# Optimization experiments

Hardware: AMD Instinct MI355X
Metric: run time of the kernel (lower is better)

## Reference

```python
import jax, jax.numpy as jnp
import numpy as np


def conv(x, w, stride=1, pad=0):
    return jax.lax.conv_general_dilated(
        x, w, (stride, stride), [(pad, pad), (pad, pad)],
        dimension_numbers=('NCHW', 'OIHW', 'NCHW'))


def group_norm(x, scale, bias, groups=32, eps=1e-5):
    B, C, H, W = x.shape
    xg = x.reshape(B, groups, C // groups, H, W)
    m = xg.mean(axis=(2, 3, 4), keepdims=True)
    v = xg.var(axis=(2, 3, 4), keepdims=True)
    xn = ((xg - m) * jax.lax.rsqrt(v + eps)).reshape(B, C, H, W)
    return xn * scale[None, :, None, None] + bias[None, :, None, None]


def bilinear_sample(x, py, px):
    # x: [B,C,H,W]; py, px: [B,K,Ho,Wo] absolute sampling coords.
    # Returns [B,C,K,Ho,Wo]; out-of-bounds corners contribute zero
    # (matches deform-conv CUDA kernel semantics).
    B, C, H, W = x.shape
    y0 = jnp.floor(py)
    x0 = jnp.floor(px)
    wy1 = py - y0
    wx1 = px - x0
    xf = x.reshape(B, C, H * W)
    Ksp = py.shape[1:]

    def corner(yi, xi, wy, wx):
        valid = (yi >= 0) & (yi < H) & (xi >= 0) & (xi < W)
        yc = jnp.clip(yi, 0, H - 1).astype(jnp.int32)
        xc = jnp.clip(xi, 0, W - 1).astype(jnp.int32)
        idx = (yc * W + xc).reshape(B, 1, -1)          # [B,1,K*Ho*Wo]
        v = jnp.take_along_axis(xf, idx, axis=2).reshape(B, C, *Ksp)
        w = (wy * wx * valid).astype(x.dtype)[:, None]  # [B,1,K,Ho,Wo]
        return v * w

    return (corner(y0, x0, 1.0 - wy1, 1.0 - wx1)
            + corner(y0, x0 + 1, 1.0 - wy1, wx1)
            + corner(y0 + 1, x0, wy1, 1.0 - wx1)
            + corner(y0 + 1, x0 + 1, wy1, wx1))


def setup_inputs() -> dict:
    key = jax.random.key(0)
    ks = jax.random.split(key, 8)
    B, Cin, H, W = 4, 1024, 64, 64
    Cb = 256  # bottleneck channels
    x = jax.random.normal(ks[0], (B, Cin, H, W), dtype=jnp.float32)
    w1 = jax.random.normal(ks[1], (Cb, Cin, 1, 1), dtype=jnp.float32) * (1.0 / np.sqrt(Cin))
    w_off = jax.random.normal(ks[2], (27, Cb, 3, 3), dtype=jnp.float32) * 0.01
    b_off = jnp.zeros((27,), dtype=jnp.float32)
    w2 = jax.random.normal(ks[3], (Cb, Cb, 3, 3), dtype=jnp.float32) * (1.0 / np.sqrt(Cb * 9))
    w3 = jax.random.normal(ks[4], (Cin, Cb, 1, 1), dtype=jnp.float32) * (1.0 / np.sqrt(Cb))
    return {
        'x': x,
        'w1': w1, 'gn1_scale': jnp.ones((Cb,), jnp.float32), 'gn1_bias': jnp.zeros((Cb,), jnp.float32),
        'w_off': w_off, 'b_off': b_off,
        'w2': w2, 'gn2_scale': jnp.ones((Cb,), jnp.float32), 'gn2_bias': jnp.zeros((Cb,), jnp.float32),
        'w3': w3, 'gn3_scale': jnp.ones((Cin,), jnp.float32), 'gn3_bias': jnp.zeros((Cin,), jnp.float32),
        'stride': 4,
    }


def reference(x, w1, gn1_scale, gn1_bias, w_off, b_off, w2, gn2_scale, gn2_bias,
              w3, gn3_scale, gn3_bias, stride):
    # stride only selects the offset-conv / norm bank (single bank here).
    out = conv(x, w1)                                   # 1x1
    out = jax.nn.relu(group_norm(out, gn1_scale, gn1_bias))

    om = conv(out, w_off, pad=1) + b_off[None, :, None, None]  # [B,27,H,W]
    K = 9
    off_x = om[:, :K]
    off_y = om[:, K:2 * K]
    mask = jax.nn.sigmoid(om[:, 2 * K:])                # [B,9,H,W]

    B, C, H, W = out.shape
    ky, kx = jnp.meshgrid(jnp.arange(3), jnp.arange(3), indexing='ij')
    ky = (ky.reshape(K) - 1).astype(om.dtype)           # kernel taps, pad=1, dil=1
    kx = (kx.reshape(K) - 1).astype(om.dtype)
    grid_y = jnp.arange(H, dtype=om.dtype)[None, :, None] + ky[:, None, None]  # [9,H,1]
    grid_x = jnp.arange(W, dtype=om.dtype)[None, None, :] + kx[:, None, None]  # [9,1,W]
    py = grid_y[None] + off_y                           # [B,9,H,W]
    px = grid_x[None] + off_x

    sampled = bilinear_sample(out, py, px) * mask[:, None]      # [B,C,9,H,W]
    out = jnp.einsum('bckhw,ock->bohw', sampled, w2.reshape(w2.shape[0], w2.shape[1], K))
    out = jax.nn.relu(group_norm(out, gn2_scale, gn2_bias))

    out = conv(out, w3)                                 # 1x1
    out = group_norm(out, gn3_scale, gn3_bias)
    return jax.nn.relu(out + x)
```

## Files before the change

### kernel.cpp

```cpp
#include <hip/hip_runtime.h>
#include <math.h>

#define BATCH 4
#define CIN   1024
#define CB    256
#define HH    64
#define WW    64
#define PP    4096
#define EPSV  1e-5f

using shortx8 = __attribute__((ext_vector_type(8))) short;
using floatx4 = __attribute__((ext_vector_type(4))) float;
using intx4   = __attribute__((ext_vector_type(4))) int;

static __device__ inline unsigned short f2bf(float f) {
    unsigned int u = __float_as_uint(f);
    u += 0x7fffu + ((u >> 16) & 1u);
    return (unsigned short)(u >> 16);
}
static __device__ inline float bf2f(unsigned short s) {
    return __uint_as_float(((unsigned int)s) << 16);
}
static __device__ inline float bflo(unsigned int u) {
    return __uint_as_float(u << 16);
}
static __device__ inline float bfhi(unsigned int u) {
    return __uint_as_float(u & 0xffff0000u);
}

__global__ __launch_bounds__(256)
void gemm_bf16(const unsigned short* __restrict__ A,
               const unsigned short* __restrict__ BTg,
               float* __restrict__ Cg, int M, int N, int K) {
    const int b = blockIdx.z;
    const unsigned short* BT = BTg + (size_t)b * N * K;
    float* C = Cg + (size_t)b * M * N;
    const int m0 = blockIdx.y * 128;
    const int n0 = blockIdx.x * 128;
    const int tid = threadIdx.x;
    const int lane = tid & 63;
    const int wid = tid >> 6;
    const int l15 = lane & 15;
    const int quad = lane >> 4;

    __shared__ __align__(16) unsigned short As[128 * 40];
    __shared__ __align__(16) unsigned short Bs[128 * 40];

    floatx4 acc[2][8];
#pragma unroll
    for (int i = 0; i < 2; i++)
#pragma unroll
        for (int j = 0; j < 8; j++) acc[i][j] = (floatx4){0.f, 0.f, 0.f, 0.f};

    const int row = tid >> 1;
    const int half = tid & 1;

    for (int k0 = 0; k0 < K; k0 += 32) {
        const unsigned short* ga = A + (size_t)(m0 + row) * K + k0 + half * 16;
        const unsigned short* gb = BT + (size_t)(n0 + row) * K + k0 + half * 16;
        float4 a0 = *(const float4*)ga;
        float4 a1 = *(const float4*)(ga + 8);
        float4 b0 = *(const float4*)gb;
        float4 b1 = *(const float4*)(gb + 8);
        __syncthreads();
        *(float4*)((char*)As + row * 80 + half * 32) = a0;
        *(float4*)((char*)As + row * 80 + half * 32 + 16) = a1;
        *(float4*)((char*)Bs + row * 80 + half * 32) = b0;
        *(float4*)((char*)Bs + row * 80 + half * 32 + 16) = b1;
        __syncthreads();
        shortx8 af[2], bf[8];
#pragma unroll
        for (int i = 0; i < 2; i++)
            af[i] = *(const shortx8*)((const char*)As +
                    (wid * 32 + 16 * i + l15) * 80 + quad * 16);
#pragma unroll
        for (int j = 0; j < 8; j++)
            bf[j] = *(const shortx8*)((const char*)Bs +
                    (16 * j + l15) * 80 + quad * 16);
#pragma unroll
        for (int i = 0; i < 2; i++)
#pragma unroll
            for (int j = 0; j < 8; j++)
                acc[i][j] = __builtin_amdgcn_mfma_f32_16x16x32_bf16(
                    af[i], bf[j], acc[i][j], 0, 0, 0);
    }

#pragma unroll
    for (int i = 0; i < 2; i++) {
#pragma unroll
        for (int r = 0; r < 4; r++) {
            int m = m0 + wid * 32 + 16 * i + quad * 4 + r;
            float* dst = C + (size_t)m * N + n0 + l15;
#pragma unroll
            for (int j = 0; j < 8; j++)
                dst[16 * j] = acc[i][j][r];
        }
    }
}

__global__ __launch_bounds__(256)
void transp_bf16(const float* __restrict__ src, unsigned short* __restrict__ dst,
                 int C, int P) {
    const int p0 = blockIdx.x * 64;
    const int c0 = blockIdx.y * 64;
    const int b = blockIdx.z;
    __shared__ unsigned short t[64][72];
    const float* s = src + ((size_t)b * C + c0) * P + p0;
    for (int e = threadIdx.x; e < 4096; e += 256) {
        int r = e >> 6, col = e & 63;
        t[r][col] = f2bf(s[(size_t)r * P + col]);
    }
    __syncthreads();
    unsigned short* d = dst + ((size_t)b * P + p0) * C + c0;
    for (int u = threadIdx.x; u < 512; u += 256) {
        int pr = u >> 3, c8 = (u & 7) * 8;
        ushort4 v0, v1;
        v0.x = t[c8 + 0][pr]; v0.y = t[c8 + 1][pr];
        v0.z = t[c8 + 2][pr]; v0.w = t[c8 + 3][pr];
        v1.x = t[c8 + 4][pr]; v1.y = t[c8 + 5][pr];
        v1.z = t[c8 + 6][pr]; v1.w = t[c8 + 7][pr];
        *(ushort4*)&d[(size_t)pr * C + c8] = v0;
        *(ushort4*)&d[(size_t)pr * C + c8 + 4] = v1;
    }
}

__global__ __launch_bounds__(256)
void gn2t(const float* __restrict__ src, const float2* __restrict__ st,
          const float* __restrict__ sc, const float* __restrict__ bi,
          unsigned short* __restrict__ dst) {
    const int p0 = blockIdx.x * 64;
    const int c0 = blockIdx.y * 64;
    const int b = blockIdx.z;
    __shared__ unsigned short t[64][72];
    const float* s = src + ((size_t)b * CB + c0) * PP + p0;
    for (int e = threadIdx.x; e < 4096; e += 256) {
        int r = e >> 6, col = e & 63;
        int c = c0 + r;
        float2 m = st[b * 32 + (c >> 3)];
        float a = m.y * sc[c];
        float bb = bi[c] - m.x * a;
        t[r][col] = f2bf(fmaxf(s[(size_t)r * PP + col] * a + bb, 0.f));
    }
    __syncthreads();
    unsigned short* d = dst + ((size_t)b * PP + p0) * CB + c0;
    for (int u = threadIdx.x; u < 512; u += 256) {
        int pr = u >> 3, c8 = (u & 7) * 8;
        ushort4 v0, v1;
        v0.x = t[c8 + 0][pr]; v0.y = t[c8 + 1][pr];
        v0.z = t[c8 + 2][pr]; v0.w = t[c8 + 3][pr];
        v1.x = t[c8 + 4][pr]; v1.y = t[c8 + 5][pr];
        v1.z = t[c8 + 6][pr]; v1.w = t[c8 + 7][pr];
        *(ushort4*)&d[(size_t)pr * CB + c8] = v0;
        *(ushort4*)&d[(size_t)pr * CB + c8 + 4] = v1;
    }
}

__global__ __launch_bounds__(256)
void cvt_bf16(const float* __restrict__ s, unsigned short* __restrict__ d, int n) {
    int i = blockIdx.x * 256 + threadIdx.x;
    if (i < n) d[i] = f2bf(s[i]);
}

__global__ __launch_bounds__(256)
void gn_stats_part(const float* __restrict__ src, float2* __restrict__ part,
                   int C, int Cpg) {
    int bgs = blockIdx.x;
    int bg = bgs >> 2, s = bgs & 3;
    int b = bg >> 5, g = bg & 31;
    const float* base = src + ((size_t)b * C + (size_t)g * Cpg) * PP;
    int n4 = (Cpg * PP) >> 2;
    int per = n4 >> 2;
    const float4* p4 = (const float4*)base + (size_t)s * per;
    float sm = 0.f, ss = 0.f;
    for (int i = threadIdx.x; i < per; i += 256) {
        float4 v = p4[i];
        sm += v.x + v.y + v.z + v.w;
        ss += v.x * v.x + v.y * v.y + v.z * v.z + v.w * v.w;
    }
    for (int off = 32; off > 0; off >>= 1) {
        sm += __shfl_down(sm, off, 64);
        ss += __shfl_down(ss, off, 64);
    }
    __shared__ float rs[4], rss[4];
    int lane = threadIdx.x & 63, wid = threadIdx.x >> 6;
    if (lane == 0) { rs[wid] = sm; rss[wid] = ss; }
    __syncthreads();
    if (threadIdx.x == 0)
        part[bgs] = make_float2(rs[0] + rs[1] + rs[2] + rs[3],
                                rss[0] + rss[1] + rss[2] + rss[3]);
}

__global__ __launch_bounds__(128)
void gn_stats_fin(const float2* __restrict__ part, float2* __restrict__ stats,
                  int cnt) {
    int bg = threadIdx.x;
    float2 p0 = part[bg * 4 + 0], p1 = part[bg * 4 + 1];
    float2 p2 = part[bg * 4 + 2], p3 = part[bg * 4 + 3];
    float S  = p0.x + p1.x + p2.x + p3.x;
    float SS = p0.y + p1.y + p2.y + p3.y;
    float mean = S / (float)cnt;
    float var = SS / (float)cnt - mean * mean;
    stats[bg] = make_float2(mean, rsqrtf(var + EPSV));
}

__global__ __launch_bounds__(256)
void woff_conv(const float* __restrict__ w_off, unsigned short* __restrict__ wobf) {
    int t = blockIdx.x * 256 + threadIdx.x;
    if (t >= 32 * 2304) return;
    int m = t / 2304;
    int r = t - m * 2304;
    int tap = r >> 8, c = r & 255;
    float v = (m < 27) ? w_off[((size_t)m * 256 + c) * 9 + tap] : 0.f;
    wobf[t] = f2bf(v);
}

__global__ __launch_bounds__(256)
void conv_off_mfma(const unsigned short* __restrict__ bfAT,
                   const unsigned short* __restrict__ wobf,
                   const float* __restrict__ boff,
                   float* __restrict__ om) {
    const int blk = blockIdx.x;
    const int xcd = blk & 7;
    const int b = xcd >> 1;
    const int tile = ((blk >> 3) << 1) | (xcd & 1);
    const int p0 = tile * 32;
    const int tid = threadIdx.x;
    const int lane = tid & 63;
    const int wid = tid >> 6;
    const int l15 = lane & 15;
    const int quad = lane >> 4;
    const int mh = (wid >> 1) << 4;
    const int ph = (wid & 1) << 4;

    __shared__ __align__(16) unsigned short Bs[8 * 1288];

    const int y0r = p0 >> 6;
    const int x0 = p0 & 63;
    const unsigned short* xb = bfAT + ((size_t)b << 20);
    const unsigned short* arow = wobf + (size_t)(mh + l15) * 2304 + quad * 8;

    floatx4 acc = (floatx4){0.f, 0.f, 0.f, 0.f};

    for (int tap = 0; tap < 9; ++tap) {
        const int dy = tap / 3 - 1, dx = tap % 3 - 1;
        const int yy = y0r + dy;
        const bool rowok = (yy >= 0 && yy < 64);
        __syncthreads();
        for (int e = tid; e < 1024; e += 256) {
            int px = e >> 5, ck = e & 31;
            int xx = x0 + px + dx;
            uint4 v = make_uint4(0u, 0u, 0u, 0u);
            if (rowok && xx >= 0 && xx < 64) {
                int srow = (yy << 6) + xx;
                v = *(const uint4*)(xb + ((size_t)srow << 8) + ck * 8);
            }
            *(uint4*)((char*)Bs + (ck >> 2) * 2576 + px * 80 + (ck & 3) * 16) = v;
        }
        __syncthreads();
        const unsigned short* at = arow + tap * 256;
#pragma unroll
        for (int cc = 0; cc < 8; ++cc) {
            shortx8 af = *(const shortx8*)(at + cc * 32);
            shortx8 bf = *(const shortx8*)((const char*)Bs + cc * 2576 +
                         (ph + l15) * 80 + quad * 16);
            acc = __builtin_amdgcn_mfma_f32_16x16x32_bf16(af, bf, acc, 0, 0, 0);
        }
    }

#pragma unroll
    for (int r = 0; r < 4; ++r) {
        int m = mh + quad * 4 + r;
        if (m < 27)
            om[((size_t)b * 27 + m) * PP + p0 + ph + l15] = acc[r] + boff[m];
    }
}

__global__ __launch_bounds__(512, 2)
void gemm2_mfma(const unsigned short* __restrict__ bfAT,
                const unsigned short* __restrict__ w2bf,
                const float* __restrict__ om, float* __restrict__ out2) {
    const int blk = blockIdx.x;
    const int xcd = blk & 7;
    const int b = xcd >> 1;
    const int p0 = (((blk >> 3) << 1) | (xcd & 1)) * 64;
    const int tid = threadIdx.x;
    const int lane = tid & 63;
    const int wid = tid >> 6;
    const int l15 = lane & 15;
    const int quad = lane >> 4;

    __shared__ __align__(16) unsigned short As0[256 * 40];
    __shared__ __align__(16) unsigned short As1[256 * 40];
    __shared__ __align__(16) unsigned short Bs0[64 * 40];
    __shared__ __align__(16) unsigned short Bs1[64 * 40];
    __shared__ float sw0[576], sw1[576], sw2[576], sw3[576];
    __shared__ int   si0[576], si1[576];

    const float* ob = om + (size_t)b * 27 * PP;
    for (int e = tid; e < 576; e += 512) {
        int k = e >> 6, p = e & 63;
        int pg = p0 + p;
        float offx = ob[(size_t)k * PP + pg];
        float offy = ob[(size_t)(9 + k) * PP + pg];
        float ms = 1.f / (1.f + expf(-ob[(size_t)(18 + k) * PP + pg]));
        int y = pg >> 6, x = pg & 63;
        float py = (float)(y + k / 3 - 1) + offy;
        float px = (float)(x + (k % 3) - 1) + offx;
        float y0f = floorf(py), x0f = floorf(px);
        float wy1 = py - y0f, wx1 = px - x0f;
        int iy0 = (int)y0f, ix0 = (int)x0f;
        int iy1 = iy0 + 1;
        float wy0v = (iy0 >= 0 && iy0 < 64) ? (1.f - wy1) * ms : 0.f;
        float wy1v = (iy1 >= 0 && iy1 < 64) ? wy1 * ms : 0.f;
        int cy0 = min(max(iy0, 0), 63), cy1 = min(max(iy1, 0), 63);
        float xa, xb; int q;
        if (ix0 >= 0 && ix0 <= 62)      { q = ix0; xa = 1.f - wx1; xb = wx1;       }
        else if (ix0 == -1)             { q = 0;   xa = wx1;       xb = 0.f;       }
        else if (ix0 == 63)             { q = 62;  xa = 0.f;       xb = 1.f - wx1; }
        else                            { q = 0;   xa = 0.f;       xb = 0.f;       }
        sw0[e] = wy0v * xa;
        sw1[e] = wy0v * xb;
        sw2[e] = wy1v * xa;
        sw3[e] = wy1v * xb;
        si0[e] = (cy0 << 6) + q;
        si1[e] = (cy1 << 6) + q;
    }

    floatx4 acc[2][4];
#pragma unroll
    for (int i = 0; i < 2; i++)
#pragma unroll
        for (int j = 0; j < 4; j++) acc[i][j] = (floatx4){0.f, 0.f, 0.f, 0.f};

    const int cq = tid & 7;
    const int bp = tid >> 3;
    const int so = tid >> 1;
    const int sh = tid & 1;
    const unsigned short* xbase = bfAT + (((size_t)b) << 20);
    const unsigned short* abase = w2bf + (size_t)so * 2304 + sh * 32;
    const unsigned short* gbq = xbase + cq * 8;
    const int mbase = wid * 32;

    __syncthreads();

    float4 a0, a1, a2, a3;
    uint4 v00, v01, v10, v11;
    float w0, w1, w2v, w3v;
    {
        a0 = ((const float4*)abase)[0];
        a1 = ((const float4*)abase)[1];
        a2 = ((const float4*)abase)[2];
        a3 = ((const float4*)abase)[3];
        int tix = bp;
        w0 = sw0[tix]; w1 = sw1[tix]; w2v = sw2[tix]; w3v = sw3[tix];
        int r0 = si0[tix], r1 = si1[tix];
        v00 = *(const uint4*)(gbq + ((size_t)r0 << 8));
        v01 = *(const uint4*)(gbq + ((size_t)(r0 + 1) << 8));
        v10 = *(const uint4*)(gbq + ((size_t)r1 << 8));
        v11 = *(const uint4*)(gbq + ((size_t)(r1 + 1) << 8));
    }

    int tap = 0, cc2 = 0;
    for (int seg = 0; seg < 36; ++seg) {
        float f0 = w0 * bflo(v00.x) + w1 * bflo(v01.x)
                 + w2v * bflo(v10.x) + w3v * bflo(v11.x);
        float f1 = w0 * bfhi(v00.x) + w1 * bfhi(v01.x)
                 + w2v * bfhi(v10.x) + w3v * bfhi(v11.x);
        float f2 = w0 * bflo(v00.y) + w1 * bflo(v01.y)
                 + w2v * bflo(v10.y) + w3v * bflo(v11.y);
        float f3 = w0 * bfhi(v00.y) + w1 * bfhi(v01.y)
                 + w2v * bfhi(v10.y) + w3v * bfhi(v11.y);
        float f4 = w0 * bflo(v00.z) + w1 * bflo(v01.z)
                 + w2v * bflo(v10.z) + w3v * bflo(v11.z);
        float f5 = w0 * bfhi(v00.z) + w1 * bfhi(v01.z)
                 + w2v * bfhi(v10.z) + w3v * bfhi(v11.z);
        float f6 = w0 * bflo(v00.w) + w1 * bflo(v01.w)
                 + w2v * bflo(v10.w) + w3v * bflo(v11.w);
        float f7 = w0 * bfhi(v00.w) + w1 * bfhi(v01.w)
                 + w2v * bfhi(v10.w) + w3v * bfhi(v11.w);
        uint4 bw;
        bw.x = (unsigned int)f2bf(f0) | ((unsigned int)f2bf(f1) << 16);
        bw.y = (unsigned int)f2bf(f2) | ((unsigned int)f2bf(f3) << 16);
        bw.z = (unsigned int)f2bf(f4) | ((unsigned int)f2bf(f5) << 16);
        bw.w = (unsigned int)f2bf(f6) | ((unsigned int)f2bf(f7) << 16);
        unsigned short* adst = sh ? As1 : As0;
        *(float4*)((char*)adst + so * 80 +  0) = a0;
        *(float4*)((char*)adst + so * 80 + 16) = a1;
        *(float4*)((char*)adst + so * 80 + 32) = a2;
        *(float4*)((char*)adst + so * 80 + 48) = a3;
        unsigned short* bdst = (cq & 4) ? Bs1 : Bs0;
        *(uint4*)((char*)bdst + bp * 80 + (cq & 3) * 16) = bw;
        __syncthreads();

        int ntap = tap + 1, ncc2 = cc2;
        if (ntap == 9) { ntap = 0; ncc2 = (cc2 + 1) & 3; }
        {
            const unsigned short* gsrc = abase + ntap * 256 + ncc2 * 64;
            a0 = ((const float4*)gsrc)[0];
            a1 = ((const float4*)gsrc)[1];
            a2 = ((const float4*)gsrc)[2];
            a3 = ((const float4*)gsrc)[3];
            int tix = ntap * 64 + bp;
            int r0 = si0[tix], r1 = si1[tix];
            const unsigned short* gb = gbq + ncc2 * 64;
            v00 = *(const uint4*)(gb + ((size_t)r0 << 8));
            v01 = *(const uint4*)(gb + ((size_t)(r0 + 1) << 8));
            v10 = *(const uint4*)(gb + ((size_t)r1 << 8));
            v11 = *(const uint4*)(gb + ((size_t)(r1 + 1) << 8));
            w0 = sw0[tix]; w1 = sw1[tix]; w2v = sw2[tix]; w3v = sw3[tix];
        }

        shortx8 af[2][2], bfr[2][4];
#pragma unroll
        for (int i = 0; i < 2; i++) {
            af[0][i] = *(const shortx8*)((const char*)As0 +
                       (mbase + 16 * i + l15) * 80 + quad * 16);
            af[1][i] = *(const shortx8*)((const char*)As1 +
                       (mbase + 16 * i + l15) * 80 + quad * 16);
        }
#pragma unroll
        for (int j = 0; j < 4; j++) {
            bfr[0][j] = *(const shortx8*)((const char*)Bs0 +
                        (16 * j + l15) * 80 + quad * 16);
            bfr[1][j] = *(const shortx8*)((const char*)Bs1 +
                        (16 * j + l15) * 80 + quad * 16);
        }
#pragma unroll
        for (int ks = 0; ks < 2; ks++)
#pragma unroll
            for (int i = 0; i < 2; i++)
#pragma unroll
                for (int j = 0; j < 4; j++)
                    acc[i][j] = __builtin_amdgcn_mfma_f32_16x16x32_bf16(
                        af[ks][i], bfr[ks][j], acc[i][j], 0, 0, 0);
        __syncthreads();
        tap = ntap; cc2 = ncc2;
    }

    const size_t chbase = ((size_t)b * CB) << 12;
#pragma unroll
    for (int i = 0; i < 2; i++) {
#pragma unroll
        for (int r = 0; r < 4; r++) {
            int row = mbase + 16 * i + quad * 4 + r;
            float* dst = out2 + chbase + ((size_t)row << 12) + p0 + l15;
#pragma unroll
            for (int j = 0; j < 4; j++)
                dst[16 * j] = acc[i][j][r];
        }
    }
}

__global__ __launch_bounds__(256)
void w2conv(const float* __restrict__ w2, unsigned short* __restrict__ w2bf) {
    int t = blockIdx.x * 256 + threadIdx.x;
    if (t >= 256 * 2304) return;
    int o = t / 2304;
    int r = t - o * 2304;
    int tap = r >> 8, c = r & 255;
    w2bf[t] = f2bf(w2[((size_t)o * 256 + c) * 9 + tap]);
}

__global__ __launch_bounds__(256)
void final_k(float* __restrict__ dout, const float* __restrict__ x,
             const float2* __restrict__ stats, const float* __restrict__ sc,
             const float* __restrict__ bi) {
    long i = (long)blockIdx.x * 256 + threadIdx.x;
    long total4 = ((long)BATCH * CIN * PP) >> 2;
    if (i >= total4) return;
    long e = i << 2;
    int c = (int)((e >> 12) & 1023);
    int b = (int)(e >> 22);
    float2 st = stats[b * 32 + (c >> 5)];
    float a = st.y * sc[c];
    float bb = bi[c] - st.x * a;
    float4 v = ((float4*)dout)[i];
    float4 xv = ((const float4*)x)[i];
    v.x = fmaxf(v.x * a + bb + xv.x, 0.f);
    v.y = fmaxf(v.y * a + bb + xv.y, 0.f);
    v.z = fmaxf(v.z * a + bb + xv.z, 0.f);
    v.w = fmaxf(v.w * a + bb + xv.w, 0.f);
    ((float4*)dout)[i] = v;
}

extern "C" void kernel_launch(void* const* d_in, const int* in_sizes, int n_in,
                              void* d_out, int out_size, void* d_ws, size_t ws_size,
                              hipStream_t stream) {
    const float* x   = (const float*)d_in[0];
    const float* w1  = (const float*)d_in[1];
    const float* g1s = (const float*)d_in[2];
    const float* g1b = (const float*)d_in[3];
    const float* wof = (const float*)d_in[4];
    const float* bof = (const float*)d_in[5];
    const float* w2  = (const float*)d_in[6];
    const float* g2s = (const float*)d_in[7];
    const float* g2b = (const float*)d_in[8];
    const float* w3  = (const float*)d_in[9];
    const float* g3s = (const float*)d_in[10];
    const float* g3b = (const float*)d_in[11];
    float* out = (float*)d_out;

    float* ws = (float*)d_ws;
    unsigned short* w1bf   = (unsigned short*)(ws + 0);
    float*          out1r  = ws + 131072;
    float*          out2   = ws + 131072;
    unsigned short* xbfT   = (unsigned short*)(ws + 4325376);
    unsigned short* bfAT   = (unsigned short*)(ws + 6422528);
    float*          om     = ws + 8519680;
    unsigned short* w2bf   = (unsigned short*)(ws + 8962048);
    unsigned short* wobf   = (unsigned short*)(ws + 9256960);
    unsigned short* out2bT = (unsigned short*)(ws + 4325376);
    unsigned short* w3bf   = (unsigned short*)(ws + 11354112);
    float2* st1  = (float2*)(ws + 11485184);
    float2* st2  = st1 + 128;
    float2* st3  = st2 + 128;
    float2* part = st3 + 128;

    transp_bf16<<<dim3(64, 16, 4), 256, 0, stream>>>(x, xbfT, 1024, 4096);
    cvt_bf16<<<1024, 256, 0, stream>>>(w1, w1bf, 262144);
    gemm_bf16<<<dim3(32, 2, 4), 256, 0, stream>>>(w1bf, xbfT, out1r, 256, 4096, 1024);
    gn_stats_part<<<512, 256, 0, stream>>>(out1r, part, 256, 8);
    gn_stats_fin<<<1, 128, 0, stream>>>(part, st1, 8 * PP);
    gn2t<<<dim3(64, 4, 4), 256, 0, stream>>>(out1r, st1, g1s, g1b, bfAT);
    woff_conv<<<288, 256, 0, stream>>>(wof, wobf);
    conv_off_mfma<<<512, 256, 0, stream>>>(bfAT, wobf, bof, om);
    w2conv<<<2304, 256, 0, stream>>>(w2, w2bf);
    cvt_bf16<<<1024, 256, 0, stream>>>(w3, w3bf, 262144);
    gemm2_mfma<<<dim3(256, 1, 1), 512, 0, stream>>>(bfAT, w2bf, om, out2);
    gn_stats_part<<<512, 256, 0, stream>>>(out2, part, 256, 8);
    gn_stats_fin<<<1, 128, 0, stream>>>(part, st2, 8 * PP);
    gn2t<<<dim3(64, 4, 4), 256, 0, stream>>>(out2, st2, g2s, g2b, out2bT);
    gemm_bf16<<<dim3(32, 8, 4), 256, 0, stream>>>(w3bf, out2bT, out, 1024, 4096, 256);
    gn_stats_part<<<512, 256, 0, stream>>>(out, part, 1024, 32);
    gn_stats_fin<<<1, 128, 0, stream>>>(part, st3, 32 * PP);
    final_k<<<16384, 256, 0, stream>>>(out, x, st3, g3s, g3b);
}
```

Baseline: 348.8 us.

## Fuse GroupNorm statistics into GEMM epilogues and load gemm2 A operand directly to registers

Result: no change. 352.1 us (+1.0%).

```diff
diff --git a/kernel.cpp b/kernel.cpp
--- a/kernel.cpp
+++ b/kernel.cpp
@@ -11,7 +11,6 @@
 
 using shortx8 = __attribute__((ext_vector_type(8))) short;
 using floatx4 = __attribute__((ext_vector_type(4))) float;
-using intx4   = __attribute__((ext_vector_type(4))) int;
 
 static __device__ inline unsigned short f2bf(float f) {
     unsigned int u = __float_as_uint(f);
@@ -31,7 +30,8 @@
 __global__ __launch_bounds__(256)
 void gemm_bf16(const unsigned short* __restrict__ A,
                const unsigned short* __restrict__ BTg,
-               float* __restrict__ Cg, int M, int N, int K) {
+               float* __restrict__ Cg, int M, int N, int K,
+               float* __restrict__ pS, float* __restrict__ pSS, int gshift) {
     const int b = blockIdx.z;
     const unsigned short* BT = BTg + (size_t)b * N * K;
     float* C = Cg + (size_t)b * M * N;
@@ -45,6 +45,8 @@
 
     __shared__ __align__(16) unsigned short As[128 * 40];
     __shared__ __align__(16) unsigned short Bs[128 * 40];
+    __shared__ float sgs[32], sgss[32];
+    if (tid < 32) { sgs[tid] = 0.f; sgss[tid] = 0.f; }
 
     floatx4 acc[2][8];
 #pragma unroll
@@ -91,10 +93,29 @@
         for (int r = 0; r < 4; r++) {
             int m = m0 + wid * 32 + 16 * i + quad * 4 + r;
             float* dst = C + (size_t)m * N + n0 + l15;
-#pragma unroll
-            for (int j = 0; j < 8; j++)
-                dst[16 * j] = acc[i][j][r];
+            float s = 0.f, ss = 0.f;
+#pragma unroll
+            for (int j = 0; j < 8; j++) {
+                float v = acc[i][j][r];
+                dst[16 * j] = v;
+                s += v; ss += v * v;
+            }
+#pragma unroll
+            for (int off = 1; off < 16; off <<= 1) {
+                s  += __shfl_xor(s, off, 64);
+                ss += __shfl_xor(ss, off, 64);
+            }
+            if (l15 == 0) {
+                int g = (m >> gshift) & 31;
+                atomicAdd(&sgs[g], s);
+                atomicAdd(&sgss[g], ss);
+            }
         }
+    }
+    __syncthreads();
+    if (tid < 32) {
+        atomicAdd(&pS[b * 32 + tid], sgs[tid]);
+        atomicAdd(&pSS[b * 32 + tid], sgss[tid]);
     }
 }
 
@@ -161,43 +182,11 @@
     if (i < n) d[i] = f2bf(s[i]);
 }
 
-__global__ __launch_bounds__(256)
-void gn_stats_part(const float* __restrict__ src, float2* __restrict__ part,
-                   int C, int Cpg) {
-    int bgs = blockIdx.x;
-    int bg = bgs >> 2, s = bgs & 3;
-    int b = bg >> 5, g = bg & 31;
-    const float* base = src + ((size_t)b * C + (size_t)g * Cpg) * PP;
-    int n4 = (Cpg * PP) >> 2;
-    int per = n4 >> 2;
-    const float4* p4 = (const float4*)base + (size_t)s * per;
-    float sm = 0.f, ss = 0.f;
-    for (int i = threadIdx.x; i < per; i += 256) {
-        float4 v = p4[i];
-        sm += v.x + v.y + v.z + v.w;
-        ss += v.x * v.x + v.y * v.y + v.z * v.z + v.w * v.w;
-    }
-    for (int off = 32; off > 0; off >>= 1) {
-        sm += __shfl_down(sm, off, 64);
-        ss += __shfl_down(ss, off, 64);
-    }
-    __shared__ float rs[4], rss[4];
-    int lane = threadIdx.x & 63, wid = threadIdx.x >> 6;
-    if (lane == 0) { rs[wid] = sm; rss[wid] = ss; }
-    __syncthreads();
-    if (threadIdx.x == 0)
-        part[bgs] = make_float2(rs[0] + rs[1] + rs[2] + rs[3],
-                                rss[0] + rss[1] + rss[2] + rss[3]);
-}
-
 __global__ __launch_bounds__(128)
-void gn_stats_fin(const float2* __restrict__ part, float2* __restrict__ stats,
-                  int cnt) {
+void gn_stats_fin(const float* __restrict__ pS, const float* __restrict__ pSS,
+                  float2* __restrict__ stats, int cnt) {
     int bg = threadIdx.x;
-    float2 p0 = part[bg * 4 + 0], p1 = part[bg * 4 + 1];
-    float2 p2 = part[bg * 4 + 2], p3 = part[bg * 4 + 3];
-    float S  = p0.x + p1.x + p2.x + p3.x;
-    float SS = p0.y + p1.y + p2.y + p3.y;
+    float S = pS[bg], SS = pSS[bg];
     float mean = S / (float)cnt;
     float var = SS / (float)cnt - mean * mean;
     stats[bg] = make_float2(mean, rsqrtf(var + EPSV));
@@ -278,7 +267,8 @@
 __global__ __launch_bounds__(512, 2)
 void gemm2_mfma(const unsigned short* __restrict__ bfAT,
                 const unsigned short* __restrict__ w2bf,
-                const float* __restrict__ om, float* __restrict__ out2) {
+                const float* __restrict__ om, float* __restrict__ out2,
+                float* __restrict__ pS, float* __restrict__ pSS) {
     const int blk = blockIdx.x;
     const int xcd = blk & 7;
     const int b = xcd >> 1;
@@ -289,12 +279,12 @@
     const int l15 = lane & 15;
     const int quad = lane >> 4;
 
-    __shared__ __align__(16) unsigned short As0[256 * 40];
-    __shared__ __align__(16) unsigned short As1[256 * 40];
     __shared__ __align__(16) unsigned short Bs0[64 * 40];
     __shared__ __align__(16) unsigned short Bs1[64 * 40];
     __shared__ float sw0[576], sw1[576], sw2[576], sw3[576];
     __shared__ int   si0[576], si1[576];
+    __shared__ float sgs[32], sgss[32];
+    if (tid < 32) { sgs[tid] = 0.f; sgss[tid] = 0.f; }
 
     const float* ob = om + (size_t)b * 27 * PP;
     for (int e = tid; e < 576; e += 512) {
@@ -334,23 +324,22 @@
 
     const int cq = tid & 7;
     const int bp = tid >> 3;
-    const int so = tid >> 1;
-    const int sh = tid & 1;
     const unsigned short* xbase = bfAT + (((size_t)b) << 20);
-    const unsigned short* abase = w2bf + (size_t)so * 2304 + sh * 32;
     const unsigned short* gbq = xbase + cq * 8;
     const int mbase = wid * 32;
+    const unsigned short* afb = w2bf + (size_t)(mbase + l15) * 2304 + quad * 8;
 
     __syncthreads();
 
-    float4 a0, a1, a2, a3;
+    shortx8 afc[2][2];
     uint4 v00, v01, v10, v11;
     float w0, w1, w2v, w3v;
     {
-        a0 = ((const float4*)abase)[0];
-        a1 = ((const float4*)abase)[1];
-        a2 = ((const float4*)abase)[2];
-        a3 = ((const float4*)abase)[3];
+#pragma unroll
+        for (int ks = 0; ks < 2; ks++)
+#pragma unroll
+            for (int i = 0; i < 2; i++)
+                afc[ks][i] = *(const shortx8*)(afb + (size_t)i * 36864 + ks * 32);
         int tix = bp;
         w0 = sw0[tix]; w1 = sw1[tix]; w2v = sw2[tix]; w3v = sw3[tix];
         int r0 = si0[tix], r1 = si1[tix];
@@ -383,23 +372,20 @@
         bw.y = (unsigned int)f2bf(f2) | ((unsigned int)f2bf(f3) << 16);
         bw.z = (unsigned int)f2bf(f4) | ((unsigned int)f2bf(f5) << 16);
         bw.w = (unsigned int)f2bf(f6) | ((unsigned int)f2bf(f7) << 16);
-        unsigned short* adst = sh ? As1 : As0;
-        *(float4*)((char*)adst + so * 80 +  0) = a0;
-        *(float4*)((char*)adst + so * 80 + 16) = a1;
-        *(float4*)((char*)adst + so * 80 + 32) = a2;
-        *(float4*)((char*)adst + so * 80 + 48) = a3;
         unsigned short* bdst = (cq & 4) ? Bs1 : Bs0;
         *(uint4*)((char*)bdst + bp * 80 + (cq & 3) * 16) = bw;
         __syncthreads();
 
         int ntap = tap + 1, ncc2 = cc2;
         if (ntap == 9) { ntap = 0; ncc2 = (cc2 + 1) & 3; }
+        shortx8 afn[2][2];
         {
-            const unsigned short* gsrc = abase + ntap * 256 + ncc2 * 64;
-            a0 = ((const float4*)gsrc)[0];
-            a1 = ((const float4*)gsrc)[1];
-            a2 = ((const float4*)gsrc)[2];
-            a3 = ((const float4*)gsrc)[3];
+            const unsigned short* ab = afb + ntap * 256 + ncc2 * 64;
+#pragma unroll
+            for (int ks = 0; ks < 2; ks++)
+#pragma unroll
+                for (int i = 0; i < 2; i++)
+                    afn[ks][i] = *(const shortx8*)(ab + (size_t)i * 36864 + ks * 32);
             int tix = ntap * 64 + bp;
             int r0 = si0[tix], r1 = si1[tix];
             const unsigned short* gb = gbq + ncc2 * 64;
@@ -410,14 +396,7 @@
             w0 = sw0[tix]; w1 = sw1[tix]; w2v = sw2[tix]; w3v = sw3[tix];
         }
 
-        shortx8 af[2][2], bfr[2][4];
-#pragma unroll
-        for (int i = 0; i < 2; i++) {
-            af[0][i] = *(const shortx8*)((const char*)As0 +
-                       (mbase + 16 * i + l15) * 80 + quad * 16);
-            af[1][i] = *(const shortx8*)((const char*)As1 +
-                       (mbase + 16 * i + l15) * 80 + quad * 16);
-        }
+        shortx8 bfr[2][4];
 #pragma unroll
         for (int j = 0; j < 4; j++) {
             bfr[0][j] = *(const shortx8*)((const char*)Bs0 +
@@ -432,8 +411,13 @@
 #pragma unroll
                 for (int j = 0; j < 4; j++)
                     acc[i][j] = __builtin_amdgcn_mfma_f32_16x16x32_bf16(
-                        af[ks][i], bfr[ks][j], acc[i][j], 0, 0, 0);
+                        afc[ks][i], bfr[ks][j], acc[i][j], 0, 0, 0);
         __syncthreads();
+#pragma unroll
+        for (int ks = 0; ks < 2; ks++)
+#pragma unroll
+            for (int i = 0; i < 2; i++)
+                afc[ks][i] = afn[ks][i];
         tap = ntap; cc2 = ncc2;
     }
 
@@ -444,10 +428,29 @@
         for (int r = 0; r < 4; r++) {
             int row = mbase + 16 * i + quad * 4 + r;
             float* dst = out2 + chbase + ((size_t)row << 12) + p0 + l15;
-#pragma unroll
-            for (int j = 0; j < 4; j++)
-                dst[16 * j] = acc[i][j][r];
+            float s = 0.f, ss = 0.f;
+#pragma unroll
+            for (int j = 0; j < 4; j++) {
+                float v = acc[i][j][r];
+                dst[16 * j] = v;
+                s += v; ss += v * v;
+            }
+#pragma unroll
+            for (int off = 1; off < 16; off <<= 1) {
+                s  += __shfl_xor(s, off, 64);
+                ss += __shfl_xor(ss, off, 64);
+            }
+            if (l15 == 0) {
+                int g = row >> 3;
+                atomicAdd(&sgs[g], s);
+                atomicAdd(&sgss[g], ss);
+            }
         }
+    }
+    __syncthreads();
+    if (tid < 32) {
+        atomicAdd(&pS[b * 32 + tid], sgs[tid]);
+        atomicAdd(&pSS[b * 32 + tid], sgss[tid]);
     }
 }
 
@@ -514,24 +517,28 @@
     float2* st1  = (float2*)(ws + 11485184);
     float2* st2  = st1 + 128;
     float2* st3  = st2 + 128;
-    float2* part = st3 + 128;
+    float*  pbuf = ws + 11485184 + 768;
+    float*  p1S = pbuf,       *p1SS = pbuf + 128;
+    float*  p2S = pbuf + 256, *p2SS = pbuf + 384;
+    float*  p3S = pbuf + 512, *p3SS = pbuf + 640;
+
+    hipMemsetAsync(pbuf, 0, 768 * sizeof(float), stream);
 
     transp_bf16<<<dim3(64, 16, 4), 256, 0, stream>>>(x, xbfT, 1024, 4096);
     cvt_bf16<<<1024, 256, 0, stream>>>(w1, w1bf, 262144);
-    gemm_bf16<<<dim3(32, 2, 4), 256, 0, stream>>>(w1bf, xbfT, out1r, 256, 4096, 1024);
-    gn_stats_part<<<512, 256, 0, stream>>>(out1r, part, 256, 8);
-    gn_stats_fin<<<1, 128, 0, stream>>>(part, st1, 8 * PP);
+    gemm_bf16<<<dim3(32, 2, 4), 256, 0, stream>>>(w1bf, xbfT, out1r, 256, 4096, 1024,
+                                                  p1S, p1SS, 3);
+    gn_stats_fin<<<1, 128, 0, stream>>>(p1S, p1SS, st1, 8 * PP);
     gn2t<<<dim3(64, 4, 4), 256, 0, stream>>>(out1r, st1, g1s, g1b, bfAT);
     woff_conv<<<288, 256, 0, stream>>>(wof, wobf);
     conv_off_mfma<<<512, 256, 0, stream>>>(bfAT, wobf, bof, om);
     w2conv<<<2304, 256, 0, stream>>>(w2, w2bf);
     cvt_bf16<<<1024, 256, 0, stream>>>(w3, w3bf, 262144);
-    gemm2_mfma<<<dim3(256, 1, 1), 512, 0, stream>>>(bfAT, w2bf, om, out2);
-    gn_stats_part<<<512, 256, 0, stream>>>(out2, part, 256, 8);
-    gn_stats_fin<<<1, 128, 0, stream>>>(part, st2, 8 * PP);
+    gemm2_mfma<<<dim3(256, 1, 1), 512, 0, stream>>>(bfAT, w2bf, om, out2, p2S, p2SS);
+    gn_stats_fin<<<1, 128, 0, stream>>>(p2S, p2SS, st2, 8 * PP);
     gn2t<<<dim3(64, 4, 4), 256, 0, stream>>>(out2, st2, g2s, g2b, out2bT);
-    gemm_bf16<<<dim3(32, 8, 4), 256, 0, stream>>>(w3bf, out2bT, out, 1024, 4096, 256);
-    gn_stats_part<<<512, 256, 0, stream>>>(out, part, 1024, 32);
-    gn_stats_fin<<<1, 128, 0, stream>>>(part, st3, 32 * PP);
+    gemm_bf16<<<dim3(32, 8, 4), 256, 0, stream>>>(w3bf, out2bT, out, 1024, 4096, 256,
+                                                  p3S, p3SS, 5);
+    gn_stats_fin<<<1, 128, 0, stream>>>(p3S, p3SS, st3, 32 * PP);
     final_k<<<16384, 256, 0, stream>>>(out, x, st3, g3s, g3b);
 }
```
